# Optimization experiments

Hardware: AMD Instinct MI355X
Metric: run time of the kernel (lower is better)

## Reference

```python
import jax, jax.numpy as jnp
import numpy as np

N_HEAD = 16

def setup_inputs() -> dict:
    key = jax.random.key(0)
    ks = jax.random.split(key, 4)
    B, S, D = 2, 2048, 2048
    return {
        "hidden_states": jax.random.normal(ks[0], (B, S, D), dtype=jnp.float32),
        "attention_mask": jnp.ones((B, S), dtype=jnp.float32),
        "W_attn": jax.random.normal(ks[1], (D, 3 * D), dtype=jnp.float32) * (D ** -0.5),
        "b_attn": jnp.zeros((3 * D,), dtype=jnp.float32),
        "W_proj": jax.random.normal(ks[2], (D, D), dtype=jnp.float32) * (D ** -0.5),
        "b_proj": jnp.zeros((D,), dtype=jnp.float32),
        "lambda_param": jnp.float32(0.8),
    }

def reference(hidden_states, attention_mask, W_attn, b_attn, W_proj, b_proj, lambda_param):
    B, S, D = hidden_states.shape
    H = N_HEAD
    hd = D // H          # full head dim (used by V and for the scale)
    qd = hd // 2         # q/k per-head dim after the dual chunk
    scale = hd ** -0.5

    qkv = hidden_states @ W_attn + b_attn            # [B,S,3D]
    q, k, v = jnp.split(qkv, 3, axis=-1)
    q1, q2 = jnp.split(q, 2, axis=-1)                # each [B,S,D/2]
    k1, k2 = jnp.split(k, 2, axis=-1)

    def heads(x, d):  # [B,S,H*d] -> [B,H,S,d]
        return x.reshape(B, S, H, d).transpose(0, 2, 1, 3)

    q1, q2 = heads(q1, qd), heads(q2, qd)
    k1, k2 = heads(k1, qd), heads(k2, qd)
    v = heads(v, hd)

    # additive mask: (1 - m) * -10000, broadcast over heads and query dim
    mask = (1.0 - attention_mask)[:, None, None, :] * -10000.0  # [B,1,1,S]

    s1 = jnp.einsum("bhqd,bhkd->bhqk", q1, k1) * scale + mask
    s2 = jnp.einsum("bhqd,bhkd->bhqk", q2, k2) * scale + mask
    w = jax.nn.softmax(s1, axis=-1) - lambda_param * jax.nn.softmax(s2, axis=-1)

    out = jnp.einsum("bhqk,bhkd->bhqd", w, v)        # [B,H,S,hd]
    out = out.transpose(0, 2, 1, 3).reshape(B, S, D)
    return out @ W_proj + b_proj
```

## Files before the change

kernel.cpp:

```cpp
#include <hip/hip_runtime.h>
#include <hip/hip_bf16.h>

typedef __attribute__((ext_vector_type(8))) short bf16x8;
typedef __attribute__((ext_vector_type(8))) unsigned short u16x8;
typedef __attribute__((ext_vector_type(4))) float f32x4;

__device__ __forceinline__ unsigned short f2bf(float f) {
  union { float f; unsigned int i; } v; v.f = f;
  unsigned int r = v.i + 0x7FFFu + ((v.i >> 16) & 1u);
  return (unsigned short)(r >> 16);
}
__device__ __forceinline__ unsigned int pack2bf_rn(float a, float b) {
  union { float f; unsigned int i; } x, y; x.f = a; y.f = b;
  return ((x.i + 0x8000u) >> 16) | ((y.i + 0x8000u) & 0xFFFF0000u);
}
__device__ __forceinline__ unsigned int cvtpk(float a, float b) {
  unsigned int r;
  asm("v_cvt_pk_bf16_f32 %0, %1, %2" : "=v"(r) : "v"(a), "v"(b));
  return r;
}
__device__ __forceinline__ float fexp2(float x) {
  float r;
  asm("v_exp_f32 %0, %1" : "=v"(r) : "v"(x));
  return r;
}
__device__ __forceinline__ void gll16(const unsigned short* g, unsigned short* l) {
  __builtin_amdgcn_global_load_lds(
      (const __attribute__((address_space(1))) unsigned int*)g,
      (__attribute__((address_space(3))) unsigned int*)l, 16, 0, 0);
}

__device__ __forceinline__ void transpose32(const float* in, unsigned short* out,
                                            long in_rs, long out_rs, int c0, int r0,
                                            unsigned short (*tile)[33]) {
  int tx = threadIdx.x & 31, ty = threadIdx.x >> 5;
#pragma unroll
  for (int i = 0; i < 32; i += 8)
    tile[ty + i][tx] = f2bf(in[(long)(r0 + ty + i) * in_rs + c0 + tx]);
  __syncthreads();
#pragma unroll
  for (int i = 0; i < 32; i += 8)
    out[(long)(c0 + ty + i) * out_rs + r0 + tx] = tile[tx][ty + i];
}

__global__ void prep_k(const float* __restrict__ hs, unsigned short* __restrict__ hsb,
                       const float* __restrict__ Wa, unsigned short* __restrict__ WtA,
                       const float* __restrict__ Wp, unsigned short* __restrict__ WtP) {
  __shared__ unsigned short tile[32][33];
  const int bid = blockIdx.x;
  if (bid < 4096) {
    long i = ((long)bid * 256 + threadIdx.x) * 8;
    float4 a = *(const float4*)(hs + i);
    float4 b = *(const float4*)(hs + i + 4);
    u16x8 o;
    o[0] = f2bf(a.x); o[1] = f2bf(a.y); o[2] = f2bf(a.z); o[3] = f2bf(a.w);
    o[4] = f2bf(b.x); o[5] = f2bf(b.y); o[6] = f2bf(b.z); o[7] = f2bf(b.w);
    *(u16x8*)(hsb + i) = o;
  } else if (bid < 16384) {
    int r = bid - 4096;
    int bx = r % 192, by = r / 192;
    transpose32(Wa, WtA, 6144, 2048, bx * 32, by * 32, tile);
  } else {
    int r = bid - 16384;
    int bx = r & 63, by = r >> 6;
    transpose32(Wp, WtP, 2048, 2048, bx * 32, by * 32, tile);
  }
}

__global__ __launch_bounds__(256) void gemm_qkv(
    const unsigned short* __restrict__ A,
    const unsigned short* __restrict__ Bt,
    const float* __restrict__ bias,
    unsigned short* __restrict__ qQ,
    unsigned short* __restrict__ k1p, unsigned short* __restrict__ k2p,
    unsigned short* __restrict__ vp) {
  const int K = 2048;
  __shared__ unsigned short As[128 * 32];
  __shared__ unsigned short Bs[128 * 32];
  const int wgid = (blockIdx.x & 7) * 192 + (blockIdx.x >> 3);
  const int m0 = (wgid / 48) * 128, n0 = (wgid % 48) * 128;
  const int tid = threadIdx.x, lane = tid & 63, wave = tid >> 6;
  const int wm = (wave >> 1) * 64, wn = (wave & 1) * 64;
  const int quad = lane >> 4, l15 = lane & 15;
  const int ar = tid >> 2, ak = (tid & 3) * 8;

  f32x4 acc[4][4] = {};
  const unsigned short* Ap = A + (long)(m0 + ar) * K + ak;
  const unsigned short* Bp = Bt + (long)(n0 + ar) * K + ak;
  unsigned short* AsW = As + wave * 512;
  unsigned short* BsW = Bs + wave * 512;

  for (int kb = 0; kb < K; kb += 32) {
    __syncthreads();
    gll16(Ap + kb, AsW);
    gll16(Ap + (long)64 * K + kb, AsW + 2048);
    gll16(Bp + kb, BsW);
    gll16(Bp + (long)64 * K + kb, BsW + 2048);
    __syncthreads();
    bf16x8 af[4], bfr[4];
#pragma unroll
    for (int t = 0; t < 4; t++)
      af[t] = *(const bf16x8*)&As[(wm + t * 16 + l15) * 32 + quad * 8];
#pragma unroll
    for (int t = 0; t < 4; t++)
      bfr[t] = *(const bf16x8*)&Bs[(wn + t * 16 + l15) * 32 + quad * 8];
#pragma unroll
    for (int i = 0; i < 4; i++)
#pragma unroll
      for (int j = 0; j < 4; j++)
        acc[i][j] = __builtin_amdgcn_mfma_f32_16x16x32_bf16(af[i], bfr[j], acc[i][j], 0, 0, 0);
  }

  const int ncol = n0 + wn;
  if (ncol < 2048) {
#pragma unroll
    for (int j = 0; j < 4; j++) {
      int n = ncol + j * 16 + l15;
      float bv = bias[n];
#pragma unroll
      for (int i = 0; i < 4; i++) {
        int mr = m0 + wm + i * 16 + quad * 4;
#pragma unroll
        for (int r = 0; r < 4; r++)
          qQ[(long)(mr + r) * 2048 + n] = f2bf(acc[i][j][r] + bv);
      }
    }
  } else if (ncol < 4096) {
    unsigned short* kp = (ncol >= 3072) ? k2p : k1p;
#pragma unroll
    for (int j = 0; j < 4; j++) {
      int n = ncol + j * 16 + l15;
      float bv = bias[n];
      int kk = (n - 2048) & 1023;
      int h = kk >> 6, c = (kk >> 3) & 7, e = kk & 7;
#pragma unroll
      for (int i = 0; i < 4; i++) {
        int mr = m0 + wm + i * 16 + quad * 4;
        int b = mr >> 11, s = mr & 2047;
        long tb2 = ((long)(b * 16 + h) * 32 + (s >> 6)) * 4096 + e;
        int row0 = s & 63;
#pragma unroll
        for (int r = 0; r < 4; r++) {
          int row = row0 + r;
          kp[tb2 + row * 64 + ((c ^ (row & 7)) << 3)] = f2bf(acc[i][j][r] + bv);
        }
      }
    }
  } else {
#pragma unroll
    for (int j = 0; j < 4; j++) {
      int n = ncol + j * 16 + l15;
      float bv = bias[n];
      int vv = n - 4096;
      int h = vv >> 7, d = vv & 127;
#pragma unroll
      for (int i = 0; i < 4; i++) {
        int mr = m0 + wm + i * 16 + quad * 4;
        int b = mr >> 11, s = mr & 2047;
        int cc = (s & 63) >> 3;
        long dst = ((long)(b * 16 + h) * 32 + (s >> 6)) * 8192 + d * 64 +
                   ((cc ^ (d & 7)) << 3) + (quad & 1) * 4;
        uint2 st;
        st.x = pack2bf_rn(acc[i][j][0] + bv, acc[i][j][1] + bv);
        st.y = pack2bf_rn(acc[i][j][2] + bv, acc[i][j][3] + bv);
        *(uint2*)&vp[dst] = st;
      }
    }
  }
}

__global__ __launch_bounds__(256) void gemm_bt_f32(
    const unsigned short* __restrict__ A,
    const unsigned short* __restrict__ Bt,
    const float* __restrict__ bias,
    float* __restrict__ C, int K, int ldc) {
  __shared__ unsigned short As[128 * 32];
  __shared__ unsigned short Bs[128 * 32];
  const int wgid = (blockIdx.x & 7) * 64 + (blockIdx.x >> 3);
  const int m0 = (wgid >> 4) * 128, n0 = (wgid & 15) * 128;
  const int tid = threadIdx.x, lane = tid & 63, wave = tid >> 6;
  const int wm = (wave >> 1) * 64, wn = (wave & 1) * 64;
  const int quad = lane >> 4, l15 = lane & 15;
  const int ar = tid >> 2, ak = (tid & 3) * 8;

  f32x4 acc[4][4] = {};
  const unsigned short* Ap = A + (long)(m0 + ar) * K + ak;
  const unsigned short* Bp = Bt + (long)(n0 + ar) * K + ak;
  unsigned short* AsW = As + wave * 512;
  unsigned short* BsW = Bs + wave * 512;

  for (int kb = 0; kb < K; kb += 32) {
    __syncthreads();
    gll16(Ap + kb, AsW);
    gll16(Ap + (long)64 * K + kb, AsW + 2048);
    gll16(Bp + kb, BsW);
    gll16(Bp + (long)64 * K + kb, BsW + 2048);
    __syncthreads();
    bf16x8 af[4], bfr[4];
#pragma unroll
    for (int t = 0; t < 4; t++)
      af[t] = *(const bf16x8*)&As[(wm + t * 16 + l15) * 32 + quad * 8];
#pragma unroll
    for (int t = 0; t < 4; t++)
      bfr[t] = *(const bf16x8*)&Bs[(wn + t * 16 + l15) * 32 + quad * 8];
#pragma unroll
    for (int i = 0; i < 4; i++)
#pragma unroll
      for (int j = 0; j < 4; j++)
        acc[i][j] = __builtin_amdgcn_mfma_f32_16x16x32_bf16(af[i], bfr[j], acc[i][j], 0, 0, 0);
  }
#pragma unroll
  for (int j = 0; j < 4; j++) {
    int n = n0 + wn + j * 16 + l15;
    float bv = bias[n];
#pragma unroll
    for (int i = 0; i < 4; i++) {
      int mr = m0 + wm + i * 16 + quad * 4;
#pragma unroll
      for (int r = 0; r < 4; r++)
        C[(long)(mr + r) * ldc + n] = acc[i][j][r] + bv;
    }
  }
}

__global__ __launch_bounds__(256, 2) void attn_k(
    const unsigned short* __restrict__ qQ,
    const unsigned short* __restrict__ k1p,
    const unsigned short* __restrict__ k2p,
    const unsigned short* __restrict__ vp,
    const float* __restrict__ mask,
    const float* __restrict__ lamp,
    unsigned short* __restrict__ out) {
  __shared__ unsigned short k1s[2 * 4096];
  __shared__ unsigned short k2s[2 * 4096];
  __shared__ unsigned short vts[2 * 8192];
  __shared__ unsigned short pls[4 * 2048];
  const int bid = blockIdx.x;
  const int wgid = (bid & 7) * 64 + (bid >> 3);
  const int bh = wgid >> 4;
  const int q0 = (wgid & 15) * 128;
  const int b = bh >> 4, h = bh & 15;
  const int tid = threadIdx.x, lane = tid & 63, wave = tid >> 6;
  const int quad = lane >> 4, l15 = lane & 15;
  const long rowq = (long)b * 2048 + q0;
  const int sw = l15 & 7;

  bf16x8 aq1[2][2], aq2[2][2];
#pragma unroll
  for (int qt = 0; qt < 2; qt++) {
    const unsigned short* qr =
        qQ + (rowq + wave * 32 + qt * 16 + l15) * 2048 + h * 64 + quad * 8;
    aq1[qt][0] = *(const bf16x8*)qr;
    aq1[qt][1] = *(const bf16x8*)(qr + 32);
    aq2[qt][0] = *(const bf16x8*)(qr + 1024);
    aq2[qt][1] = *(const bf16x8*)(qr + 1056);
  }
  f32x4 o1[2][8] = {}, o2[2][8] = {};
  f32x4 l1a[2] = {}, l2a[2] = {};
  bf16x8 ones;
#pragma unroll
  for (int e = 0; e < 8; e++) ones[e] = (short)0x3F80;
  const float SL = 0.08838834764831845f * 1.4426950408889634f;
  const float ML = 1.4426950408889634e4f;
  const long tb = (long)bh * 32;
  unsigned short* pw = pls + wave * 2048;

  {
    const unsigned short* k1t = k1p + tb * 4096 + tid * 8;
    const unsigned short* k2t = k2p + tb * 4096 + tid * 8;
    const unsigned short* vtt = vp + tb * 8192 + tid * 8;
    gll16(k1t, k1s + wave * 512);
    gll16(k1t + 2048, k1s + 2048 + wave * 512);
    gll16(k2t, k2s + wave * 512);
    gll16(k2t + 2048, k2s + 2048 + wave * 512);
#pragma unroll
    for (int rr = 0; rr < 4; rr++)
      gll16(vtt + rr * 2048, vts + rr * 2048 + wave * 512);
  }

  for (int t = 0; t < 32; t++) {
    const int cb = t & 1;
    __syncthreads();
    float4 mq[4];
#pragma unroll
    for (int nt = 0; nt < 4; nt++)
      mq[nt] = *(const float4*)(mask + (long)b * 2048 + t * 64 + nt * 16 + quad * 4);
    if (t < 31) {
      const unsigned short* k1t = k1p + (tb + t + 1) * 4096 + tid * 8;
      const unsigned short* k2t = k2p + (tb + t + 1) * 4096 + tid * 8;
      const unsigned short* vtt = vp + (tb + t + 1) * 8192 + tid * 8;
      unsigned short* d1 = k1s + (cb ^ 1) * 4096 + wave * 512;
      unsigned short* d2 = k2s + (cb ^ 1) * 4096 + wave * 512;
      unsigned short* dv = vts + (cb ^ 1) * 8192 + wave * 512;
      gll16(k1t, d1);
      gll16(k1t + 2048, d1 + 2048);
      gll16(k2t, d2);
      gll16(k2t + 2048, d2 + 2048);
#pragma unroll
      for (int rr = 0; rr < 4; rr++)
        gll16(vtt + rr * 2048, dv + rr * 2048);
    }

#pragma unroll
    for (int half = 0; half < 2; half++) {
      f32x4 s1[2][2] = {}, s2[2][2] = {};
#pragma unroll
      for (int np = 0; np < 2; np++) {
        const int row = cb * 4096 + (half * 32 + np * 16 + l15) * 64;
#pragma unroll
        for (int ks = 0; ks < 2; ks++) {
          const int p = ((ks * 4 + quad) ^ sw) * 8;
          bf16x8 kf1 = *(const bf16x8*)&k1s[row + p];
          bf16x8 kf2 = *(const bf16x8*)&k2s[row + p];
#pragma unroll
          for (int qt = 0; qt < 2; qt++) {
            s1[qt][np] = __builtin_amdgcn_mfma_f32_16x16x32_bf16(kf1, aq1[qt][ks], s1[qt][np], 0, 0, 0);
            s2[qt][np] = __builtin_amdgcn_mfma_f32_16x16x32_bf16(kf2, aq2[qt][ks], s2[qt][np], 0, 0, 0);
          }
        }
      }
      float ma[2][4];
#pragma unroll
      for (int np = 0; np < 2; np++)
#pragma unroll
        for (int r = 0; r < 4; r++)
          ma[np][r] = fmaf(((const float*)&mq[half * 2 + np])[r], ML, -ML);
#pragma unroll
      for (int qt = 0; qt < 2; qt++)
#pragma unroll
        for (int np = 0; np < 2; np++) {
          const int addr = l15 * 32 + (((np * 4 + quad) ^ sw) << 2);
          uint2 w1, w2;
          w1.x = cvtpk(fexp2(fmaf(s1[qt][np][0], SL, ma[np][0])),
                       fexp2(fmaf(s1[qt][np][1], SL, ma[np][1])));
          w1.y = cvtpk(fexp2(fmaf(s1[qt][np][2], SL, ma[np][2])),
                       fexp2(fmaf(s1[qt][np][3], SL, ma[np][3])));
          w2.x = cvtpk(fexp2(fmaf(s2[qt][np][0], SL, ma[np][0])),
                       fexp2(fmaf(s2[qt][np][1], SL, ma[np][1])));
          w2.y = cvtpk(fexp2(fmaf(s2[qt][np][2], SL, ma[np][2])),
                       fexp2(fmaf(s2[qt][np][3], SL, ma[np][3])));
          *(uint2*)&pw[(qt * 2 + 0) * 512 + addr] = w1;
          *(uint2*)&pw[(qt * 2 + 1) * 512 + addr] = w2;
        }
      bf16x8 f1[2], f2[2];
      {
        const int ra = l15 * 32 + (((quad * 2 + 0) ^ sw) << 2);
        const int rb = l15 * 32 + (((quad * 2 + 1) ^ sw) << 2);
#pragma unroll
        for (int qt = 0; qt < 2; qt++) {
          union { bf16x8 v; uint2 u2[2]; } g1, g2;
          g1.u2[0] = *(const uint2*)&pw[(qt * 2 + 0) * 512 + ra];
          g1.u2[1] = *(const uint2*)&pw[(qt * 2 + 0) * 512 + rb];
          g2.u2[0] = *(const uint2*)&pw[(qt * 2 + 1) * 512 + ra];
          g2.u2[1] = *(const uint2*)&pw[(qt * 2 + 1) * 512 + rb];
          f1[qt] = g1.v; f2[qt] = g2.v;
        }
      }
#pragma unroll
      for (int qt = 0; qt < 2; qt++) {
        l1a[qt] = __builtin_amdgcn_mfma_f32_16x16x32_bf16(ones, f1[qt], l1a[qt], 0, 0, 0);
        l2a[qt] = __builtin_amdgcn_mfma_f32_16x16x32_bf16(ones, f2[qt], l2a[qt], 0, 0, 0);
      }
#pragma unroll
      for (int dn = 0; dn < 8; dn++) {
        const int pp = ((half * 4 + quad) ^ sw) * 8;
        bf16x8 vf = *(const bf16x8*)&vts[cb * 8192 + (dn * 16 + l15) * 64 + pp];
#pragma unroll
        for (int qt = 0; qt < 2; qt++) {
          o1[qt][dn] = __builtin_amdgcn_mfma_f32_16x16x32_bf16(vf, f1[qt], o1[qt][dn], 0, 0, 0);
          o2[qt][dn] = __builtin_amdgcn_mfma_f32_16x16x32_bf16(vf, f2[qt], o2[qt][dn], 0, 0, 0);
        }
      }
    }
  }
  float lam = lamp[0];
#pragma unroll
  for (int qt = 0; qt < 2; qt++) {
    float i1 = 1.f / l1a[qt][0], i2 = lam / l2a[qt][0];
    unsigned short* orow =
        out + (rowq + wave * 32 + qt * 16 + l15) * 2048 + h * 128 + quad * 4;
#pragma unroll
    for (int dn = 0; dn < 8; dn++) {
      uint2 st;
      st.x = cvtpk(o1[qt][dn][0] * i1 - o2[qt][dn][0] * i2,
                   o1[qt][dn][1] * i1 - o2[qt][dn][1] * i2);
      st.y = cvtpk(o1[qt][dn][2] * i1 - o2[qt][dn][2] * i2,
                   o1[qt][dn][3] * i1 - o2[qt][dn][3] * i2);
      *(uint2*)(orow + dn * 16) = st;
    }
  }
}

extern "C" void kernel_launch(void* const* d_in, const int* in_sizes, int n_in,
                              void* d_out, int out_size, void* d_ws, size_t ws_size,
                              hipStream_t stream) {
  (void)in_sizes; (void)n_in; (void)out_size; (void)ws_size;
  const float* hs   = (const float*)d_in[0];
  const float* mask = (const float*)d_in[1];
  const float* Wa   = (const float*)d_in[2];
  const float* ba   = (const float*)d_in[3];
  const float* Wp   = (const float*)d_in[4];
  const float* bp   = (const float*)d_in[5];
  const float* lam  = (const float*)d_in[6];
  float* out = (float*)d_out;
  unsigned short* ws = (unsigned short*)d_ws;

  unsigned short* hsb = ws;
  unsigned short* WtA = hsb + (long)4096 * 2048;
  unsigned short* WtP = WtA + (long)6144 * 2048;
  unsigned short* qQ  = WtP + (long)2048 * 2048;
  unsigned short* K1p = qQ + (long)4096 * 2048;
  unsigned short* K2p = K1p + (long)2 * 16 * 2048 * 64;
  unsigned short* Vp  = K2p + (long)2 * 16 * 2048 * 64;
  unsigned short* att = hsb;

  prep_k<<<20480, 256, 0, stream>>>(hs, hsb, Wa, WtA, Wp, WtP);
  gemm_qkv<<<1536, 256, 0, stream>>>(hsb, WtA, ba, qQ, K1p, K2p, Vp);
  attn_k<<<512, 256, 0, stream>>>(qQ, K1p, K2p, Vp, mask, lam, att);
  gemm_bt_f32<<<512, 256, 0, stream>>>(att, WtP, bp, out, 2048, 2048);
}
```

Measured before the change: 449.1 us.

## Double GEMM K-tile to 64 with XOR-swizzled LDS and 2D grid

```diff
diff --git a/kernel.cpp b/kernel.cpp
--- a/kernel.cpp
+++ b/kernel.cpp
@@ -67,6 +67,7 @@
   }
 }
 
+
 __global__ __launch_bounds__(256) void gemm_qkv(
     const unsigned short* __restrict__ A,
     const unsigned short* __restrict__ Bt,
@@ -75,40 +76,45 @@
     unsigned short* __restrict__ k1p, unsigned short* __restrict__ k2p,
     unsigned short* __restrict__ vp) {
   const int K = 2048;
-  __shared__ unsigned short As[128 * 32];
-  __shared__ unsigned short Bs[128 * 32];
-  const int wgid = (blockIdx.x & 7) * 192 + (blockIdx.x >> 3);
-  const int m0 = (wgid / 48) * 128, n0 = (wgid % 48) * 128;
+  __shared__ unsigned short As[128 * 64];
+  __shared__ unsigned short Bs[128 * 64];
+  const int m0 = blockIdx.y * 128, n0 = blockIdx.x * 128;
   const int tid = threadIdx.x, lane = tid & 63, wave = tid >> 6;
   const int wm = (wave >> 1) * 64, wn = (wave & 1) * 64;
   const int quad = lane >> 4, l15 = lane & 15;
-  const int ar = tid >> 2, ak = (tid & 3) * 8;
+  const int sw = l15 & 7;
+  const int arow = wave * 8 + (lane >> 3);
+  const int acol = ((lane & 7) ^ ((lane >> 3) & 7)) * 8;
 
   f32x4 acc[4][4] = {};
-  const unsigned short* Ap = A + (long)(m0 + ar) * K + ak;
-  const unsigned short* Bp = Bt + (long)(n0 + ar) * K + ak;
+  const unsigned short* Ap = A + (long)(m0 + arow) * K + acol;
+  const unsigned short* Bp = Bt + (long)(n0 + arow) * K + acol;
   unsigned short* AsW = As + wave * 512;
   unsigned short* BsW = Bs + wave * 512;
 
-  for (int kb = 0; kb < K; kb += 32) {
+  for (int kb = 0; kb < K; kb += 64) {
     __syncthreads();
-    gll16(Ap + kb, AsW);
-    gll16(Ap + (long)64 * K + kb, AsW + 2048);
-    gll16(Bp + kb, BsW);
-    gll16(Bp + (long)64 * K + kb, BsW + 2048);
+#pragma unroll
+    for (int s = 0; s < 4; s++) {
+      gll16(Ap + s * 32 * K + kb, AsW + s * 2048);
+      gll16(Bp + s * 32 * K + kb, BsW + s * 2048);
+    }
     __syncthreads();
-    bf16x8 af[4], bfr[4];
-#pragma unroll
-    for (int t = 0; t < 4; t++)
-      af[t] = *(const bf16x8*)&As[(wm + t * 16 + l15) * 32 + quad * 8];
-#pragma unroll
-    for (int t = 0; t < 4; t++)
-      bfr[t] = *(const bf16x8*)&Bs[(wn + t * 16 + l15) * 32 + quad * 8];
-#pragma unroll
-    for (int i = 0; i < 4; i++)
-#pragma unroll
-      for (int j = 0; j < 4; j++)
-        acc[i][j] = __builtin_amdgcn_mfma_f32_16x16x32_bf16(af[i], bfr[j], acc[i][j], 0, 0, 0);
+#pragma unroll
+    for (int ks = 0; ks < 2; ks++) {
+      bf16x8 af[4], bfr[4];
+#pragma unroll
+      for (int t = 0; t < 4; t++)
+        af[t] = *(const bf16x8*)&As[(wm + t * 16 + l15) * 64 + (((ks * 4 + quad) ^ sw) << 3)];
+#pragma unroll
+      for (int t = 0; t < 4; t++)
+        bfr[t] = *(const bf16x8*)&Bs[(wn + t * 16 + l15) * 64 + (((ks * 4 + quad) ^ sw) << 3)];
+#pragma unroll
+      for (int i = 0; i < 4; i++)
+#pragma unroll
+        for (int j = 0; j < 4; j++)
+          acc[i][j] = __builtin_amdgcn_mfma_f32_16x16x32_bf16(af[i], bfr[j], acc[i][j], 0, 0, 0);
+    }
   }
 
   const int ncol = n0 + wn;
@@ -174,40 +180,45 @@
     const unsigned short* __restrict__ Bt,
     const float* __restrict__ bias,
     float* __restrict__ C, int K, int ldc) {
-  __shared__ unsigned short As[128 * 32];
-  __shared__ unsigned short Bs[128 * 32];
-  const int wgid = (blockIdx.x & 7) * 64 + (blockIdx.x >> 3);
-  const int m0 = (wgid >> 4) * 128, n0 = (wgid & 15) * 128;
+  __shared__ unsigned short As[128 * 64];
+  __shared__ unsigned short Bs[128 * 64];
+  const int m0 = blockIdx.y * 128, n0 = blockIdx.x * 128;
   const int tid = threadIdx.x, lane = tid & 63, wave = tid >> 6;
   const int wm = (wave >> 1) * 64, wn = (wave & 1) * 64;
   const int quad = lane >> 4, l15 = lane & 15;
-  const int ar = tid >> 2, ak = (tid & 3) * 8;
+  const int sw = l15 & 7;
+  const int arow = wave * 8 + (lane >> 3);
+  const int acol = ((lane & 7) ^ ((lane >> 3) & 7)) * 8;
 
   f32x4 acc[4][4] = {};
-  const unsigned short* Ap = A + (long)(m0 + ar) * K + ak;
-  const unsigned short* Bp = Bt + (long)(n0 + ar) * K + ak;
+  const unsigned short* Ap = A + (long)(m0 + arow) * K + acol;
+  const unsigned short* Bp = Bt + (long)(n0 + arow) * K + acol;
   unsigned short* AsW = As + wave * 512;
   unsigned short* BsW = Bs + wave * 512;
 
-  for (int kb = 0; kb < K; kb += 32) {
+  for (int kb = 0; kb < K; kb += 64) {
     __syncthreads();
-    gll16(Ap + kb, AsW);
-    gll16(Ap + (long)64 * K + kb, AsW + 2048);
-    gll16(Bp + kb, BsW);
-    gll16(Bp + (long)64 * K + kb, BsW + 2048);
+#pragma unroll
+    for (int s = 0; s < 4; s++) {
+      gll16(Ap + (long)s * 32 * K + kb, AsW + s * 2048);
+      gll16(Bp + (long)s * 32 * K + kb, BsW + s * 2048);
+    }
     __syncthreads();
-    bf16x8 af[4], bfr[4];
-#pragma unroll
-    for (int t = 0; t < 4; t++)
-      af[t] = *(const bf16x8*)&As[(wm + t * 16 + l15) * 32 + quad * 8];
-#pragma unroll
-    for (int t = 0; t < 4; t++)
-      bfr[t] = *(const bf16x8*)&Bs[(wn + t * 16 + l15) * 32 + quad * 8];
-#pragma unroll
-    for (int i = 0; i < 4; i++)
-#pragma unroll
-      for (int j = 0; j < 4; j++)
-        acc[i][j] = __builtin_amdgcn_mfma_f32_16x16x32_bf16(af[i], bfr[j], acc[i][j], 0, 0, 0);
+#pragma unroll
+    for (int ks = 0; ks < 2; ks++) {
+      bf16x8 af[4], bfr[4];
+#pragma unroll
+      for (int t = 0; t < 4; t++)
+        af[t] = *(const bf16x8*)&As[(wm + t * 16 + l15) * 64 + (((ks * 4 + quad) ^ sw) << 3)];
+#pragma unroll
+      for (int t = 0; t < 4; t++)
+        bfr[t] = *(const bf16x8*)&Bs[(wn + t * 16 + l15) * 64 + (((ks * 4 + quad) ^ sw) << 3)];
+#pragma unroll
+      for (int i = 0; i < 4; i++)
+#pragma unroll
+        for (int j = 0; j < 4; j++)
+          acc[i][j] = __builtin_amdgcn_mfma_f32_16x16x32_bf16(af[i], bfr[j], acc[i][j], 0, 0, 0);
+    }
   }
 #pragma unroll
   for (int j = 0; j < 4; j++) {
@@ -415,7 +426,7 @@
   unsigned short* att = hsb;
 
   prep_k<<<20480, 256, 0, stream>>>(hs, hsb, Wa, WtA, Wp, WtP);
-  gemm_qkv<<<1536, 256, 0, stream>>>(hsb, WtA, ba, qQ, K1p, K2p, Vp);
+  gemm_qkv<<<dim3(48, 32), 256, 0, stream>>>(hsb, WtA, ba, qQ, K1p, K2p, Vp);
   attn_k<<<512, 256, 0, stream>>>(qQ, K1p, K2p, Vp, mask, lam, att);
-  gemm_bt_f32<<<512, 256, 0, stream>>>(att, WtP, bp, out, 2048, 2048);
-}
+  gemm_bt_f32<<<dim3(16, 32), 256, 0, stream>>>(att, WtP, bp, out, 2048, 2048);
+}
```

After: 401.2 us. -10.7%, faster.
